# Kernel optimization log

Measured on AMD Instinct MI355X. Metric: run time of the kernel, lower is better.

Reference implementation:

```python
import jax, jax.numpy as jnp
import numpy as np

LAMBDA = 0.2
BETA = 1.0
EPS = 1e-6


def setup_inputs() -> dict:
    key = jax.random.key(0)
    t_prime = jax.random.normal(key, (8192, 768), dtype=jnp.float32)
    return {"t_prime": t_prime}


def reference(t_prime) -> jnp.ndarray:
    vocab = t_prime.shape[0]
    # L2-normalize rows (matches F.normalize p=2, dim=1 with its 1e-12 clamp)
    norm = jnp.maximum(jnp.linalg.norm(t_prime, axis=1, keepdims=True), 1e-12)
    t_norm = t_prime / norm
    # [vocab, vocab] cosine similarity
    S = t_norm @ t_norm.T
    diag = jnp.diagonal(S)
    collapse = jnp.sum((diag - 1.0) ** 2)
    # HNS path: off-diagonal entries per row, expressed without boolean reshape.
    # neg_sims = S with diagonal removed; reweight * neg^2 = beta * neg^3 / (mean_neg + eps)
    S_off = S - jnp.diag(diag)  # zero diagonal == off-diagonal values
    mean_neg = jnp.sum(S_off, axis=1) / (vocab - 1)  # per-row mean of negatives
    row_cube = jnp.sum(S_off ** 3, axis=1)  # diagonal contributes 0
    hard_neg_loss = BETA * jnp.sum(row_cube / (mean_neg + EPS))
    return collapse + LAMBDA * hard_neg_loss
```

## Files before the change

kernel.cpp:

```cpp
#include <hip/hip_runtime.h>
#include <math.h>

#define VV 8192
#define DD 768
#define NDMAX 256

typedef __attribute__((ext_vector_type(8))) short bf16x8;
typedef __attribute__((ext_vector_type(4))) float f32x4;

__device__ inline ushort f2bf(float f) {
    uint u = __float_as_uint(f);
    uint r = (u + 0x7fffu + ((u >> 16) & 1u)) >> 16;
    return (ushort)r;
}
__device__ inline float bf2f(ushort h) { return __uint_as_float(((uint)h) << 16); }

__device__ inline void gload16(const ushort* g, ushort* l) {
    __builtin_amdgcn_global_load_lds(
        (const __attribute__((address_space(1))) void*)g,
        (__attribute__((address_space(3))) void*)l, 16, 0, 0);
}

__global__ __launch_bounds__(256) void k_normpack(const float* __restrict__ t,
                                                  float* __restrict__ norms,
                                                  ushort* __restrict__ xh,
                                                  ushort* __restrict__ xl,
                                                  float* __restrict__ rc,
                                                  int* __restrict__ dlist,
                                                  int* __restrict__ dcount) {
    int r = blockIdx.x;
    const float* tr = t + (size_t)r * DD;
    int tid = threadIdx.x;
    float v0 = tr[tid], v1 = tr[tid + 256], v2 = tr[tid + 512];
    double s = (double)v0 * v0 + (double)v1 * v1 + (double)v2 * v2;
#pragma unroll
    for (int o = 32; o > 0; o >>= 1) s += __shfl_down(s, o, 64);
    __shared__ double wsum[4];
    int lane = tid & 63, w = tid >> 6;
    if (lane == 0) wsum[w] = s;
    __syncthreads();
    double tot = wsum[0] + wsum[1] + wsum[2] + wsum[3];
    float norm = fmaxf((float)sqrt(tot), 1e-12f);
    if (tid == 0) {
        norms[r] = norm;
        rc[r] = 0.f;
    }
    if (r == 0) {
        dlist[tid] = -1;
        if (tid == 0) *dcount = 0;
    }
    size_t base = (size_t)r * DD;
#pragma unroll
    for (int q = 0; q < 3; ++q) {
        int k = tid + q * 256;
        float v = (q == 0 ? v0 : (q == 1 ? v1 : v2)) / norm;
        ushort h = f2bf(v);
        xh[base + k] = h;
        xl[base + k] = f2bf(v - bf2f(h));
    }
}

__global__ __launch_bounds__(256) void k_colsumA(const float* __restrict__ t,
                                                 const float* __restrict__ norms,
                                                 double* __restrict__ gp) {
    int k = threadIdx.x;
    int r0 = blockIdx.x * 32;
    double s0 = 0.0, s1 = 0.0, s2 = 0.0;
    for (int r = r0; r < r0 + 32; ++r) {
        const float* tr = t + (size_t)r * DD;
        float nrm = norms[r];
        s0 += (double)(tr[k] / nrm);
        s1 += (double)(tr[k + 256] / nrm);
        s2 += (double)(tr[k + 512] / nrm);
    }
    double* gb = gp + (size_t)blockIdx.x * DD;
    gb[k] = s0;
    gb[k + 256] = s1;
    gb[k + 512] = s2;
}

__global__ __launch_bounds__(256) void k_colsumB(const double* __restrict__ gp,
                                                 double* __restrict__ g) {
    __shared__ double red[8][32];
    int c = threadIdx.x & 31, part = threadIdx.x >> 5;
    int col = blockIdx.x * 32 + c;
    double s = 0.0;
    for (int b = part * 32; b < part * 32 + 32; ++b)
        s += gp[(size_t)b * DD + col];
    red[part][c] = s;
    __syncthreads();
    if (part == 0) {
        double tt = 0.0;
        for (int p = 0; p < 8; ++p) tt += red[p][c];
        g[col] = tt;
    }
}

__global__ __launch_bounds__(256) void k_mean(const float* __restrict__ t,
                                              const float* __restrict__ norms,
                                              const double* __restrict__ g,
                                              double* __restrict__ mnum,
                                              double* __restrict__ dd,
                                              int* __restrict__ dlist,
                                              int* __restrict__ dcount) {
    int r = blockIdx.x * 4 + (threadIdx.x >> 6);
    int lane = threadIdx.x & 63;
    const float* tr = t + (size_t)r * DD;
    float nrm = norms[r];
    double xg = 0.0, xx = 0.0;
#pragma unroll
    for (int k = lane; k < DD; k += 64) {
        float xf = tr[k] / nrm;
        double xv = (double)xf;
        xg += xv * g[k];
        xx += xv * xv;
    }
#pragma unroll
    for (int o = 32; o > 0; o >>= 1) {
        xg += __shfl_down(xg, o, 64);
        xx += __shfl_down(xx, o, 64);
    }
    if (lane == 0) {
        double m = xg - xx;
        mnum[r] = m;
        dd[r] = xx;
        if (fabs(m / 8191.0 + 1e-6) < 1e-5) {
            int pos = atomicAdd(dcount, 1);
            if (pos < NDMAX) dlist[pos] = r;
        }
    }
}

__global__ __launch_bounds__(256, 2) void k_cube(const ushort* __restrict__ xh,
                                                 const ushort* __restrict__ xl,
                                                 const int* __restrict__ dlist,
                                                 float* __restrict__ Sb,
                                                 float* __restrict__ rc) {
    __shared__ ushort As0[4096], As1[4096], As2[4096];
    __shared__ ushort Bs0[8192], Bs1[8192], Bs2[8192];

    const int bid = blockIdx.x;
    const int tid = threadIdx.x;
    const int lane = tid & 63;
    const int wid = tid >> 6;
    const int l15 = lane & 15, li4 = lane >> 4;
    const int wm = wid >> 1, wn = wid & 1;

    const bool strip = (bid < 192);
    int bi = 0, bj = 0, seg = 0, rp = 0, cp = 0;
    if (strip) {
        seg = bid >> 6;
        int rem = bid & 63;
        rp = rem >> 5;
        cp = rem & 31;
    } else {
        int idx = bid - 192;
        int wg = (idx & 7) * 132 + (idx >> 3);
        int j = 0;
        while (wg >= 2 * j + 2) { wg -= 2 * j + 2; ++j; }
        bi = wg;
        bj = j;
    }
    const ushort* XA = strip ? ((seg == 1) ? xl : xh) : xh;
    const ushort* XB = strip ? ((seg == 2) ? xl : xh) : xh;

    int asrc[2], bsrc[4], lda_[2], ldb_[4];
#pragma unroll
    for (int j = 0; j < 2; ++j) {
        int li = tid + j * 256;
        int row = li >> 2;
        int sl = ((li & 3) ^ ((li >> 3) & 3)) * 8;
        int ar = strip ? dlist[rp * 128 + row] : (bi * 128 + row);
        if (ar < 0) ar = 0;
        asrc[j] = ar * DD + sl;
        lda_[j] = li * 8;
    }
#pragma unroll
    for (int j = 0; j < 4; ++j) {
        int li = tid + j * 256;
        int row = li >> 2;
        int sl = ((li & 3) ^ ((li >> 3) & 3)) * 8;
        int br = strip ? (cp * 256 + row) : (bj * 256 + row);
        bsrc[j] = br * DD + sl;
        ldb_[j] = li * 8;
    }

    const int swz = (li4 ^ ((l15 >> 1) & 3)) << 3;
    const int aoff = (wm * 64 + l15) * 32 + swz;
    const int boff = (wn * 128 + l15) * 32 + swz;

    f32x4 acc[4][8];
#pragma unroll
    for (int f = 0; f < 4; ++f)
#pragma unroll
        for (int n = 0; n < 8; ++n) acc[f][n] = (f32x4){0.f, 0.f, 0.f, 0.f};

#define STG(AW, BW, KT)                                  \
    do {                                                 \
        const int kq_ = (KT) * 32;                       \
        gload16(XA + asrc[0] + kq_, (AW) + lda_[0]);     \
        gload16(XA + asrc[1] + kq_, (AW) + lda_[1]);     \
        gload16(XB + bsrc[0] + kq_, (BW) + ldb_[0]);     \
        gload16(XB + bsrc[1] + kq_, (BW) + ldb_[1]);     \
        gload16(XB + bsrc[2] + kq_, (BW) + ldb_[2]);     \
        gload16(XB + bsrc[3] + kq_, (BW) + ldb_[3]);     \
    } while (0)

#define COMPUTE(AR, BR)                                                     \
    do {                                                                    \
        bf16x8 av[4], bv[8];                                                \
        _Pragma("unroll") for (int f = 0; f < 4; ++f)                       \
            av[f] = *(const bf16x8*)((AR) + aoff + f * 512);                \
        _Pragma("unroll") for (int n = 0; n < 8; ++n)                       \
            bv[n] = *(const bf16x8*)((BR) + boff + n * 512);                \
        _Pragma("unroll") for (int f = 0; f < 4; ++f)                       \
            _Pragma("unroll") for (int n = 0; n < 8; ++n)                   \
                acc[f][n] = __builtin_amdgcn_mfma_f32_16x16x32_bf16(        \
                    av[f], bv[n], acc[f][n], 0, 0, 0);                      \
    } while (0)

#define VMW6() asm volatile("s_waitcnt vmcnt(6)" ::: "memory")
#define VMW0() asm volatile("s_waitcnt vmcnt(0)" ::: "memory")
#define RBAR() asm volatile("s_barrier" ::: "memory")

    STG(As0, Bs0, 0);
    STG(As1, Bs1, 1);
    VMW6(); RBAR();

    for (int tb = 0; tb < 21; tb += 3) {
        STG(As2, Bs2, tb + 2);
        COMPUTE(As0, Bs0);
        VMW6(); RBAR();
        STG(As0, Bs0, tb + 3);
        COMPUTE(As1, Bs1);
        VMW6(); RBAR();
        STG(As1, Bs1, tb + 4);
        COMPUTE(As2, Bs2);
        VMW6(); RBAR();
    }
    STG(As2, Bs2, 23);
    COMPUTE(As0, Bs0);
    VMW6(); RBAR();
    COMPUTE(As1, Bs1);
    VMW0(); RBAR();
    COMPUTE(As2, Bs2);
#undef STG
#undef COMPUTE
#undef VMW6
#undef VMW0
#undef RBAR

    if (strip) {
#pragma unroll
        for (int f = 0; f < 4; ++f)
#pragma unroll
            for (int n = 0; n < 8; ++n)
#pragma unroll
                for (int r = 0; r < 4; ++r) {
                    int slot = seg * 256 + rp * 128 + wm * 64 + f * 16 + li4 * 4 + r;
                    int col = cp * 256 + wn * 128 + n * 16 + l15;
                    Sb[((size_t)slot << 13) + col] = acc[f][n][r];
                }
        return;
    }

    const bool dtile = ((bi >> 1) == bj);
    const int R0 = bi * 128, C0 = bj * 256;
    float rsum[4][4], csum[8];
#pragma unroll
    for (int n = 0; n < 8; ++n) csum[n] = 0.f;
#pragma unroll
    for (int f = 0; f < 4; ++f)
#pragma unroll
        for (int r = 0; r < 4; ++r) rsum[f][r] = 0.f;
#pragma unroll
    for (int f = 0; f < 4; ++f)
#pragma unroll
        for (int n = 0; n < 8; ++n)
#pragma unroll
            for (int r = 0; r < 4; ++r) {
                float s = acc[f][n][r];
                float c = s * s * s;
                int ri = R0 + wm * 64 + f * 16 + li4 * 4 + r;
                int cj = C0 + wn * 128 + n * 16 + l15;
                if (dtile && ri == cj) c = 0.f;
                rsum[f][r] += c;
                csum[n] += c;
            }
#pragma unroll
    for (int o = 1; o < 16; o <<= 1)
#pragma unroll
        for (int f = 0; f < 4; ++f)
#pragma unroll
            for (int r = 0; r < 4; ++r)
                rsum[f][r] += __shfl_xor(rsum[f][r], o, 64);
    if (l15 == 0) {
#pragma unroll
        for (int f = 0; f < 4; ++f)
#pragma unroll
            for (int r = 0; r < 4; ++r)
                atomicAdd(&rc[R0 + wm * 64 + f * 16 + li4 * 4 + r], rsum[f][r]);
    }
    if (!dtile) {
#pragma unroll
        for (int o = 16; o < 64; o <<= 1)
#pragma unroll
            for (int n = 0; n < 8; ++n) csum[n] += __shfl_xor(csum[n], o, 64);
        if (li4 == 0) {
#pragma unroll
            for (int n = 0; n < 8; ++n)
                atomicAdd(&rc[C0 + wn * 128 + n * 16 + l15], csum[n]);
        }
    }
}

__global__ __launch_bounds__(256) void k_cubefin(const float* __restrict__ Sb,
                                                 const int* __restrict__ dlist,
                                                 float* __restrict__ rc) {
    const int slot = blockIdx.x;
    const int drow = dlist[slot];
    if (drow < 0) return;
    const int tid = threadIdx.x;
    const float* s0p = Sb + ((size_t)slot << 13);
    const float* s1p = Sb + ((size_t)(256 + slot) << 13);
    const float* s2p = Sb + ((size_t)(512 + slot) << 13);
    float sum = 0.f;
    for (int c = tid; c < VV; c += 256) {
        float s0 = s0p[c];
        float sf = s0 + s1p[c] + s2p[c];
        float d = sf * sf * sf - s0 * s0 * s0;
        if (c == drow) d = 0.f;
        sum += d;
    }
    __shared__ float red[256];
    red[tid] = sum;
    __syncthreads();
    for (int o = 128; o > 0; o >>= 1) {
        if (tid < o) red[tid] += red[tid + o];
        __syncthreads();
    }
    if (tid == 0) atomicAdd(&rc[drow], red[0]);
}

__global__ __launch_bounds__(1024) void k_final(const float* __restrict__ rc,
                                                const double* __restrict__ mnum,
                                                const double* __restrict__ dd,
                                                float* __restrict__ out) {
    int tid = threadIdx.x;
    double acc = 0.0, col = 0.0;
    for (int r = tid; r < VV; r += 1024) {
        double m = mnum[r] / 8191.0 + 1e-6;
        acc += (double)rc[r] / m;
        double dm = dd[r] - 1.0;
        col += dm * dm;
    }
    __shared__ double sa[1024], sc[1024];
    sa[tid] = acc;
    sc[tid] = col;
    __syncthreads();
    for (int o = 512; o > 0; o >>= 1) {
        if (tid < o) {
            sa[tid] += sa[tid + o];
            sc[tid] += sc[tid + o];
        }
        __syncthreads();
    }
    if (tid == 0) out[0] = (float)(sc[0] + 0.2 * sa[0]);
}

extern "C" void kernel_launch(void* const* d_in, const int* in_sizes, int n_in,
                              void* d_out, int out_size, void* d_ws, size_t ws_size,
                              hipStream_t stream) {
    const float* t = (const float*)d_in[0];
    float* out = (float*)d_out;

    char* ws = (char*)d_ws;
    float* Sb = (float*)ws;
    size_t off = (size_t)VV * DD * sizeof(float);
    ushort* xh = (ushort*)(ws + off); off += (size_t)VV * DD * sizeof(ushort);
    ushort* xl = (ushort*)(ws + off); off += (size_t)VV * DD * sizeof(ushort);
    double* g = (double*)(ws + off);  off += DD * sizeof(double);
    double* mnum = (double*)(ws + off); off += VV * sizeof(double);
    double* dd = (double*)(ws + off);  off += VV * sizeof(double);
    float* rc = (float*)(ws + off);    off += VV * sizeof(float);
    int* dlist = (int*)(ws + off);     off += NDMAX * sizeof(int);
    int* dcount = (int*)(ws + off);    off += sizeof(int) + 60;
    float* norms = (float*)(ws + off); off += VV * sizeof(float);
    double* gp = (double*)(ws + off);  off += (size_t)256 * DD * sizeof(double);

    k_normpack<<<VV, 256, 0, stream>>>(t, norms, xh, xl, rc, dlist, dcount);
    k_colsumA<<<256, 256, 0, stream>>>(t, norms, gp);
    k_colsumB<<<24, 256, 0, stream>>>(gp, g);
    k_mean<<<VV / 4, 256, 0, stream>>>(t, norms, g, mnum, dd, dlist, dcount);
    k_cube<<<1248, 256, 0, stream>>>(xh, xl, dlist, Sb, rc);
    k_cubefin<<<NDMAX, 256, 0, stream>>>(Sb, dlist, rc);
    k_final<<<1, 1024, 0, stream>>>(rc, mnum, dd, out);
}
```

Baseline: 133.5 us.

## Fuse row normalization with column-sum partials and skip empty strip blocks

Merges the per-row normalize/pack kernel and the column-sum partial kernel into one kernel where each block handles 16 rows, computing norms, bf16 hi/lo splits and per-column partial sums in a single pass over the input. This removes a second full read of the input matrix and one launch, at the cost of fewer, longer blocks (512 instead of 8192). The colsumB reduction is widened to 512 partials to match. The strip blocks in the cube kernel now exit early when their dlist slot is empty.

```diff
diff --git a/kernel.cpp b/kernel.cpp
--- a/kernel.cpp
+++ b/kernel.cpp
@@ -21,62 +21,63 @@
         (__attribute__((address_space(3))) void*)l, 16, 0, 0);
 }
 
-__global__ __launch_bounds__(256) void k_normpack(const float* __restrict__ t,
-                                                  float* __restrict__ norms,
-                                                  ushort* __restrict__ xh,
-                                                  ushort* __restrict__ xl,
-                                                  float* __restrict__ rc,
-                                                  int* __restrict__ dlist,
-                                                  int* __restrict__ dcount) {
-    int r = blockIdx.x;
-    const float* tr = t + (size_t)r * DD;
-    int tid = threadIdx.x;
-    float v0 = tr[tid], v1 = tr[tid + 256], v2 = tr[tid + 512];
-    double s = (double)v0 * v0 + (double)v1 * v1 + (double)v2 * v2;
-#pragma unroll
-    for (int o = 32; o > 0; o >>= 1) s += __shfl_down(s, o, 64);
-    __shared__ double wsum[4];
-    int lane = tid & 63, w = tid >> 6;
-    if (lane == 0) wsum[w] = s;
-    __syncthreads();
-    double tot = wsum[0] + wsum[1] + wsum[2] + wsum[3];
-    float norm = fmaxf((float)sqrt(tot), 1e-12f);
-    if (tid == 0) {
-        norms[r] = norm;
-        rc[r] = 0.f;
-    }
-    if (r == 0) {
+__global__ __launch_bounds__(256) void k_normfused(const float* __restrict__ t,
+                                                   float* __restrict__ norms,
+                                                   ushort* __restrict__ xh,
+                                                   ushort* __restrict__ xl,
+                                                   double* __restrict__ gp,
+                                                   float* __restrict__ rc,
+                                                   int* __restrict__ dlist,
+                                                   int* __restrict__ dcount) {
+    const int tid = threadIdx.x;
+    const int r0 = blockIdx.x * 16;
+    if (tid < 16) rc[r0 + tid] = 0.f;
+    if (blockIdx.x == 0) {
         dlist[tid] = -1;
         if (tid == 0) *dcount = 0;
     }
-    size_t base = (size_t)r * DD;
-#pragma unroll
-    for (int q = 0; q < 3; ++q) {
-        int k = tid + q * 256;
-        float v = (q == 0 ? v0 : (q == 1 ? v1 : v2)) / norm;
-        ushort h = f2bf(v);
-        xh[base + k] = h;
-        xl[base + k] = f2bf(v - bf2f(h));
-    }
-}
-
-__global__ __launch_bounds__(256) void k_colsumA(const float* __restrict__ t,
-                                                 const float* __restrict__ norms,
-                                                 double* __restrict__ gp) {
-    int k = threadIdx.x;
-    int r0 = blockIdx.x * 32;
+    __shared__ double wsum[2][4];
+    const int lane = tid & 63, w = tid >> 6;
     double s0 = 0.0, s1 = 0.0, s2 = 0.0;
-    for (int r = r0; r < r0 + 32; ++r) {
-        const float* tr = t + (size_t)r * DD;
-        float nrm = norms[r];
-        s0 += (double)(tr[k] / nrm);
-        s1 += (double)(tr[k + 256] / nrm);
-        s2 += (double)(tr[k + 512] / nrm);
+    for (int rr = 0; rr < 16; rr += 2) {
+        const float* trA = t + (size_t)(r0 + rr) * DD;
+        const float* trB = trA + DD;
+        float a0 = trA[tid], a1 = trA[tid + 256], a2 = trA[tid + 512];
+        float b0 = trB[tid], b1 = trB[tid + 256], b2 = trB[tid + 512];
+        double sA = (double)a0 * a0 + (double)a1 * a1 + (double)a2 * a2;
+        double sB = (double)b0 * b0 + (double)b1 * b1 + (double)b2 * b2;
+#pragma unroll
+        for (int o = 32; o > 0; o >>= 1) {
+            sA += __shfl_down(sA, o, 64);
+            sB += __shfl_down(sB, o, 64);
+        }
+        if (lane == 0) { wsum[0][w] = sA; wsum[1][w] = sB; }
+        __syncthreads();
+        float nA = fmaxf((float)sqrt(wsum[0][0] + wsum[0][1] + wsum[0][2] + wsum[0][3]), 1e-12f);
+        float nB = fmaxf((float)sqrt(wsum[1][0] + wsum[1][1] + wsum[1][2] + wsum[1][3]), 1e-12f);
+        __syncthreads();
+        if (tid == 0) {
+            norms[r0 + rr] = nA;
+            norms[r0 + rr + 1] = nB;
+        }
+        size_t baseA = (size_t)(r0 + rr) * DD, baseB = baseA + DD;
+        float xA0 = a0 / nA, xA1 = a1 / nA, xA2 = a2 / nA;
+        float xB0 = b0 / nB, xB1 = b1 / nB, xB2 = b2 / nB;
+        ushort h;
+        h = f2bf(xA0); xh[baseA + tid] = h;       xl[baseA + tid] = f2bf(xA0 - bf2f(h));
+        h = f2bf(xA1); xh[baseA + tid + 256] = h; xl[baseA + tid + 256] = f2bf(xA1 - bf2f(h));
+        h = f2bf(xA2); xh[baseA + tid + 512] = h; xl[baseA + tid + 512] = f2bf(xA2 - bf2f(h));
+        h = f2bf(xB0); xh[baseB + tid] = h;       xl[baseB + tid] = f2bf(xB0 - bf2f(h));
+        h = f2bf(xB1); xh[baseB + tid + 256] = h; xl[baseB + tid + 256] = f2bf(xB1 - bf2f(h));
+        h = f2bf(xB2); xh[baseB + tid + 512] = h; xl[baseB + tid + 512] = f2bf(xB2 - bf2f(h));
+        s0 += (double)xA0; s0 += (double)xB0;
+        s1 += (double)xA1; s1 += (double)xB1;
+        s2 += (double)xA2; s2 += (double)xB2;
     }
     double* gb = gp + (size_t)blockIdx.x * DD;
-    gb[k] = s0;
-    gb[k + 256] = s1;
-    gb[k + 512] = s2;
+    gb[tid] = s0;
+    gb[tid + 256] = s1;
+    gb[tid + 512] = s2;
 }
 
 __global__ __launch_bounds__(256) void k_colsumB(const double* __restrict__ gp,
@@ -85,7 +86,7 @@
     int c = threadIdx.x & 31, part = threadIdx.x >> 5;
     int col = blockIdx.x * 32 + c;
     double s = 0.0;
-    for (int b = part * 32; b < part * 32 + 32; ++b)
+    for (int b = part * 64; b < part * 64 + 64; ++b)
         s += gp[(size_t)b * DD + col];
     red[part][c] = s;
     __syncthreads();
@@ -153,6 +154,7 @@
         int rem = bid & 63;
         rp = rem >> 5;
         cp = rem & 31;
+        if (dlist[rp * 128] < 0) return;
     } else {
         int idx = bid - 192;
         int wg = (idx & 7) * 132 + (idx >> 3);
@@ -386,10 +388,9 @@
     int* dlist = (int*)(ws + off);     off += NDMAX * sizeof(int);
     int* dcount = (int*)(ws + off);    off += sizeof(int) + 60;
     float* norms = (float*)(ws + off); off += VV * sizeof(float);
-    double* gp = (double*)(ws + off);  off += (size_t)256 * DD * sizeof(double);
-
-    k_normpack<<<VV, 256, 0, stream>>>(t, norms, xh, xl, rc, dlist, dcount);
-    k_colsumA<<<256, 256, 0, stream>>>(t, norms, gp);
+    double* gp = (double*)(ws + off);  off += (size_t)512 * DD * sizeof(double);
+
+    k_normfused<<<512, 256, 0, stream>>>(t, norms, xh, xl, gp, rc, dlist, dcount);
     k_colsumB<<<24, 256, 0, stream>>>(gp, g);
     k_mean<<<VV / 4, 256, 0, stream>>>(t, norms, g, mnum, dd, dlist, dcount);
     k_cube<<<1248, 256, 0, stream>>>(xh, xl, dlist, Sb, rc);
```

Measured after the change: 121.1 us (median of 2 runs). 9.4% less time.
